# Optimization experiments

Measured on AMD Instinct MI355X. Metric: run time of the kernel, lower is better.

## Reference

```python
import jax, jax.numpy as jnp
import numpy as np

HEADS = 16
HEAD_DIM = 64

def setup_inputs() -> dict:
    key = jax.random.key(0)
    ks = jax.random.split(key, 5)
    S, B, H = 1024, 4, 1024
    scale = 1.0 / np.sqrt(H)
    return {
        "hidden_states": jax.random.normal(ks[0], (S, B, H), jnp.float32),
        "attention_mask": jnp.zeros((B * HEADS, 1, S), jnp.float32),
        "Wq": jax.random.normal(ks[1], (H, H), jnp.float32) * scale,
        "bq": jnp.zeros((H,), jnp.float32),
        "Wk": jax.random.normal(ks[2], (H, H), jnp.float32) * scale,
        "bk": jnp.zeros((H,), jnp.float32),
        "Wv": jax.random.normal(ks[3], (H, H), jnp.float32) * scale,
        "bv": jnp.zeros((H,), jnp.float32),
    }

def reference(hidden_states, attention_mask, Wq, bq, Wk, bk, Wv, bv):
    S, B, H = hidden_states.shape
    d = HEAD_DIM
    inv_sqrt_d = 1.0 / np.sqrt(d)
    # QKV projections (torch Linear: x @ W.T + b)
    q = hidden_states @ Wq.T + bq  # (S, B, H)
    k = hidden_states @ Wk.T + bk
    v = hidden_states @ Wv.T + bv
    # (S, B*heads, d) -> (B*heads, S, d)
    q = q.reshape(S, B * HEADS, d).transpose(1, 0, 2)
    k = k.reshape(S, B * HEADS, d).transpose(1, 0, 2)
    v = v.reshape(S, B * HEADS, d).transpose(1, 0, 2)
    # SDDMM: scaled scores + additive mask -> (B*heads, S, S)
    scores = jnp.einsum('nsd,ntd->nst', q, k) * inv_sqrt_d + attention_mask
    probs = jax.nn.softmax(scores, axis=-1)
    # AV bmm -> (B*heads, S, d); note: dropout in source is seeded but never applied
    ctx = jnp.einsum('nst,ntd->nsd', probs, v)
    # back to (S, B, hidden)
    ctx = ctx.transpose(1, 0, 2).reshape(S, B, H)
    return ctx
```

## Files before the change

kernel.cpp:

```cpp
#include <hip/hip_runtime.h>
#include <hip/hip_bf16.h>
#include <math.h>

#define S_LEN 1024
#define BATCH 4
#define HID 1024
#define NHEADS 16
#define DHEAD 64
#define NTOT 64
#define M_ROWS 4096

typedef unsigned short u16;
typedef unsigned int u32;
typedef __bf16 bf16x8 __attribute__((ext_vector_type(8)));
typedef float f32x4 __attribute__((ext_vector_type(4)));

__device__ __forceinline__ u16 f2bf(float x) {
    __hip_bfloat16 h = __float2bfloat16(x);
    return *(u16*)&h;
}

__device__ __forceinline__ float fexp2(float x) {
#if __has_builtin(__builtin_amdgcn_exp2f)
    return __builtin_amdgcn_exp2f(x);
#else
    return __expf(x * 0.6931471805599453f);
#endif
}

__device__ __forceinline__ u32 cvtpk(float a, float b) {
    u32 r;
    asm("v_cvt_pk_bf16_f32 %0, %1, %2" : "=v"(r) : "v"(a), "v"(b));
    return r;
}

__device__ __forceinline__ void pl16swap(u32& a, u32& b) {
    asm("v_permlane16_swap_b32 %0, %1" : "+v"(a), "+v"(b));
}

__device__ __forceinline__ void gll16(const u16* g, u16* l) {
    __builtin_amdgcn_global_load_lds(
        (const __attribute__((address_space(1))) u32*)g,
        (__attribute__((address_space(3))) u32*)l, 16, 0, 0);
}

__global__ __launch_bounds__(256) void cvt_all(
    const float* __restrict__ X, const float* __restrict__ wq,
    const float* __restrict__ wk, const float* __restrict__ wv,
    u16* __restrict__ Xb, u16* __restrict__ Wb)
{
    const int bid = blockIdx.x;
    const float* src;
    u16* dst;
    size_t off;
    if (bid < 4096) {
        src = X; dst = Xb; off = (size_t)bid * 1024;
    } else {
        const int wb = bid - 4096;
        const int which = wb >> 10;
        src = (which == 0) ? wq : (which == 1) ? wk : wv;
        dst = Wb + (size_t)which * HID * HID;
        off = (size_t)(wb & 1023) * 1024;
    }
    const size_t idx = off + threadIdx.x * 4;
    float4 x = *(const float4*)(src + idx);
    *(ushort4*)(dst + idx) = make_ushort4(f2bf(x.x), f2bf(x.y), f2bf(x.z), f2bf(x.w));
}

__global__ __launch_bounds__(256, 3) void qkv_mfma(
    const u16* __restrict__ Xb, const u16* __restrict__ Wb,
    const float* __restrict__ bq, const float* __restrict__ bk,
    const float* __restrict__ bv,
    u16* __restrict__ Qb, u16* __restrict__ Kb, u16* __restrict__ VT)
{
    const int m0 = blockIdx.x * 128;
    const int n0 = blockIdx.y * 128;
    const int which = blockIdx.z;

    __shared__ __align__(16) u16 As[128 * 64];
    __shared__ __align__(16) u16 Bs[128 * 64];

    const int tid = threadIdx.x;
    const int lane = tid & 63;
    const int w = tid >> 6;
    const int wm = w & 1, wn = w >> 1;
    const int quad = lane >> 4;
    const int l15 = lane & 15;
    const int r7 = l15 & 7;

    const u16* W = Wb + (size_t)which * HID * HID;

    f32x4 acc[4][4];
    #pragma unroll
    for (int i = 0; i < 4; ++i)
        #pragma unroll
        for (int j = 0; j < 4; ++j)
            #pragma unroll
            for (int r = 0; r < 4; ++r) acc[i][j][r] = 0.0f;

    const int srow = lane >> 3;
    const int scg  = ((lane & 7) ^ srow) * 8;

    for (int k0 = 0; k0 < HID; k0 += 64) {
        #pragma unroll
        for (int c = 0; c < 4; ++c) {
            const int seg = w * 4 + c;
            const int row = seg * 8 + srow;
            gll16(Xb + (size_t)(m0 + row) * HID + k0 + scg, As + seg * 512);
            gll16(W  + (size_t)(n0 + row) * HID + k0 + scg, Bs + seg * 512);
        }
        __syncthreads();

        #pragma unroll
        for (int kk = 0; kk < 2; ++kk) {
            const int xo = ((kk * 4 + quad) ^ r7) * 8;
            bf16x8 af[4], bf[4];
            #pragma unroll
            for (int i = 0; i < 4; ++i)
                af[i] = *(const bf16x8*)(As + (wm * 64 + i * 16 + l15) * 64 + xo);
            #pragma unroll
            for (int j = 0; j < 4; ++j)
                bf[j] = *(const bf16x8*)(Bs + (wn * 64 + j * 16 + l15) * 64 + xo);
            #pragma unroll
            for (int i = 0; i < 4; ++i)
                #pragma unroll
                for (int j = 0; j < 4; ++j)
                    acc[i][j] = __builtin_amdgcn_mfma_f32_16x16x32_bf16(
                        af[i], bf[j], acc[i][j], 0, 0, 0);
        }
        __syncthreads();
    }

    const float* bias = (which == 0) ? bq : (which == 1) ? bk : bv;
    #pragma unroll
    for (int j = 0; j < 4; ++j) {
        const int o = n0 + wn * 64 + j * 16 + l15;
        const float bias_v = bias[o];
        const int head = o >> 6, d = o & 63;
        #pragma unroll
        for (int i = 0; i < 4; ++i) {
            const int mbase = m0 + wm * 64 + i * 16 + quad * 4;
            const int s = mbase >> 2;
            #pragma unroll
            for (int r = 0; r < 4; ++r) {
                const int n = r * NHEADS + head;
                const u16 hv = f2bf(acc[i][j][r] + bias_v);
                if (which == 0)
                    Qb[((size_t)n * S_LEN + s) * DHEAD + d] = hv;
                else if (which == 1)
                    Kb[((size_t)n * S_LEN + s) * DHEAD + d] = hv;
                else
                    VT[(size_t)n * (DHEAD * S_LEN) + (size_t)d * S_LEN + s] = hv;
            }
        }
    }
}

__global__ __launch_bounds__(256, 2) void attn_mfma(
    const u16* __restrict__ Qb, const u16* __restrict__ Kb,
    const u16* __restrict__ VT, const float* __restrict__ mask,
    float* __restrict__ out)
{
    const int bid = blockIdx.x;
    const int swz = (bid & 7) * 64 + (bid >> 3);
    const int n = swz >> 3;
    const int s0 = (swz & 7) * 128;
    const int b = n >> 4, head = n & 15;

    __shared__ __align__(16) char smem[69632];
    u16* Kbuf = (u16*)smem;
    u16* Vbuf = (u16*)(smem + 32768);
    float* Ms = (float*)(smem + 65536);
    float* Of = (float*)smem;

    const int tid = threadIdx.x;
    const int lane = tid & 63;
    const int w = tid >> 6;
    const int quad = lane >> 4;
    const int l15 = lane & 15;
    const int r7 = l15 & 7;
    const size_t nbase = (size_t)n * S_LEN * DHEAD;

    const float LOG2E = 1.44269504f;
    const float SCL2  = 0.18033688f;
    const float MOFF  = -23.0831099f;

    const int xs0 = ((quad ^ r7) * 8);
    const int xs1 = (((4 + quad) ^ r7) * 8);
    const int qperm = ((quad & 1) << 1) | (quad >> 1);
    const int xv0 = ((qperm ^ r7) * 8);
    const int xv1 = (((4 + qperm) ^ r7) * 8);

    const int srow = lane >> 3;
    const int scg  = (lane & 7) ^ (srow & 7);

    {
        float4 mv = *(const float4*)(mask + (size_t)n * S_LEN + tid * 4);
        Ms[tid * 4 + 0] = fmaf(mv.x, LOG2E, MOFF);
        Ms[tid * 4 + 1] = fmaf(mv.y, LOG2E, MOFF);
        Ms[tid * 4 + 2] = fmaf(mv.z, LOG2E, MOFF);
        Ms[tid * 4 + 3] = fmaf(mv.w, LOG2E, MOFF);
    }

    bf16x8 qf[2][2];
    #pragma unroll
    for (int mi = 0; mi < 2; ++mi)
        #pragma unroll
        for (int st = 0; st < 2; ++st)
            qf[mi][st] = *(const bf16x8*)(Qb + nbase +
                (size_t)(s0 + w * 32 + mi * 16 + l15) * 64 + st * 32 + quad * 8);

    f32x4 O[2][4];
    float l_lane[2];
    #pragma unroll
    for (int mi = 0; mi < 2; ++mi) {
        l_lane[mi] = 0.0f;
        #pragma unroll
        for (int jt = 0; jt < 4; ++jt)
            #pragma unroll
            for (int r = 0; r < 4; ++r) O[mi][jt][r] = 0.0f;
    }

    {
        #pragma unroll
        for (int h = 0; h < 2; ++h) {
            #pragma unroll
            for (int c = 0; c < 2; ++c) {
                const int seg = w * 2 + c;
                const int row = seg * 8 + srow;
                gll16(Kb + nbase + (size_t)(h * 64 + row) * 64 + scg * 8,
                      Kbuf + h * 4096 + seg * 512);
                gll16(VT + nbase + (size_t)row * S_LEN + h * 64 + scg * 8,
                      Vbuf + h * 4096 + seg * 512);
            }
        }
    }
    __syncthreads();

    u32 pw[2][2][2][4];

    for (int it = 0; it < 8; ++it) {
        const int t0 = it * 128;
        const u16* kb = Kbuf + (it & 1) * 8192;
        const u16* vb = Vbuf + (it & 1) * 8192;

        if (it < 7) {
            u16* kd = Kbuf + ((it + 1) & 1) * 8192;
            u16* vd = Vbuf + ((it + 1) & 1) * 8192;
            const int t0n = t0 + 128;
            #pragma unroll
            for (int h = 0; h < 2; ++h) {
                #pragma unroll
                for (int c = 0; c < 2; ++c) {
                    const int seg = w * 2 + c;
                    const int row = seg * 8 + srow;
                    gll16(Kb + nbase + (size_t)(t0n + h * 64 + row) * 64 + scg * 8,
                          kd + h * 4096 + seg * 512);
                    gll16(VT + nbase + (size_t)row * S_LEN + t0n + h * 64 + scg * 8,
                          vd + h * 4096 + seg * 512);
                }
            }
        }

        #pragma unroll
        for (int h = 0; h < 2; ++h) {
            const u16* kbh = kb + h * 4096;

            f32x4 sc[2][4];
            #pragma unroll
            for (int mi = 0; mi < 2; ++mi)
                #pragma unroll
                for (int j = 0; j < 4; ++j)
                    #pragma unroll
                    for (int r = 0; r < 4; ++r) sc[mi][j][r] = 0.0f;

            __builtin_amdgcn_s_setprio(1);
            #pragma unroll
            for (int st = 0; st < 2; ++st) {
                const int xo = st ? xs1 : xs0;
                bf16x8 kf[4];
                #pragma unroll
                for (int j = 0; j < 4; ++j)
                    kf[j] = *(const bf16x8*)(kbh + (j * 16 + l15) * 64 + xo);
                #pragma unroll
                for (int mi = 0; mi < 2; ++mi)
                    #pragma unroll
                    for (int j = 0; j < 4; ++j)
                        sc[mi][j] = __builtin_amdgcn_mfma_f32_16x16x32_bf16(
                            kf[j], qf[mi][st], sc[mi][j], 0, 0, 0);
            }
            __builtin_amdgcn_s_setprio(0);

            float4 mb4[4];
            #pragma unroll
            for (int j = 0; j < 4; ++j)
                mb4[j] = *(const float4*)(Ms + t0 + h * 64 + j * 16 + quad * 4);

            #pragma unroll
            for (int mi = 0; mi < 2; ++mi) {
                float pj[4][4];
                #pragma unroll
                for (int j = 0; j < 4; ++j) {
                    pj[j][0] = fexp2(fmaf(sc[mi][j][0], SCL2, mb4[j].x));
                    pj[j][1] = fexp2(fmaf(sc[mi][j][1], SCL2, mb4[j].y));
                    pj[j][2] = fexp2(fmaf(sc[mi][j][2], SCL2, mb4[j].z));
                    pj[j][3] = fexp2(fmaf(sc[mi][j][3], SCL2, mb4[j].w));
                    l_lane[mi] += (pj[j][0] + pj[j][1]) + (pj[j][2] + pj[j][3]);
                }
                u32 W00 = cvtpk(pj[0][0], pj[0][1]), W01 = cvtpk(pj[0][2], pj[0][3]);
                u32 W10 = cvtpk(pj[1][0], pj[1][1]), W11 = cvtpk(pj[1][2], pj[1][3]);
                u32 W20 = cvtpk(pj[2][0], pj[2][1]), W21 = cvtpk(pj[2][2], pj[2][3]);
                u32 W30 = cvtpk(pj[3][0], pj[3][1]), W31 = cvtpk(pj[3][2], pj[3][3]);
                pl16swap(W00, W10); pl16swap(W01, W11);
                pl16swap(W20, W30); pl16swap(W21, W31);
                pw[mi][h][0][0] = W00; pw[mi][h][0][1] = W01;
                pw[mi][h][0][2] = W10; pw[mi][h][0][3] = W11;
                pw[mi][h][1][0] = W20; pw[mi][h][1][1] = W21;
                pw[mi][h][1][2] = W30; pw[mi][h][1][3] = W31;
            }
        }

        __builtin_amdgcn_s_setprio(1);
        #pragma unroll
        for (int h = 0; h < 2; ++h) {
            const u16* vbh = vb + h * 4096;
            #pragma unroll
            for (int st = 0; st < 2; ++st) {
                const int xo = st ? xv1 : xv0;
                bf16x8 vf[4];
                #pragma unroll
                for (int jt = 0; jt < 4; ++jt)
                    vf[jt] = *(const bf16x8*)(vbh + (jt * 16 + l15) * 64 + xo);
                #pragma unroll
                for (int mi = 0; mi < 2; ++mi) {
                    union { u32 wds[4]; bf16x8 v; } pu;
                    pu.wds[0] = pw[mi][h][st][0]; pu.wds[1] = pw[mi][h][st][1];
                    pu.wds[2] = pw[mi][h][st][2]; pu.wds[3] = pw[mi][h][st][3];
                    #pragma unroll
                    for (int jt = 0; jt < 4; ++jt)
                        O[mi][jt] = __builtin_amdgcn_mfma_f32_16x16x32_bf16(
                            vf[jt], pu.v, O[mi][jt], 0, 0, 0);
                }
            }
        }
        __builtin_amdgcn_s_setprio(0);

        __syncthreads();
    }

    float inv_l[2];
    #pragma unroll
    for (int mi = 0; mi < 2; ++mi) {
        float l = l_lane[mi];
        l += __shfl_xor(l, 16);
        l += __shfl_xor(l, 32);
        inv_l[mi] = 1.0f / l;
    }
    __syncthreads();

    #pragma unroll
    for (int mi = 0; mi < 2; ++mi) {
        const int q = w * 32 + mi * 16 + l15;
        #pragma unroll
        for (int jt = 0; jt < 4; ++jt)
            #pragma unroll
            for (int r = 0; r < 4; ++r)
                Of[q * 72 + jt * 16 + quad * 4 + r] = O[mi][jt][r] * inv_l[mi];
    }
    __syncthreads();

    const int tx = tid & 15, ty = tid >> 4;
    #pragma unroll
    for (int p = 0; p < 8; ++p) {
        const int q = p * 16 + ty;
        float4 v = *(const float4*)(Of + q * 72 + tx * 4);
        *(float4*)(out + (size_t)(s0 + q) * (BATCH * HID) + (size_t)b * HID +
                   head * DHEAD + tx * 4) = v;
    }
}

extern "C" void kernel_launch(void* const* d_in, const int* in_sizes, int n_in,
                              void* d_out, int out_size, void* d_ws, size_t ws_size,
                              hipStream_t stream)
{
    const float* X    = (const float*)d_in[0];
    const float* mask = (const float*)d_in[1];
    const float* Wq   = (const float*)d_in[2];
    const float* bq   = (const float*)d_in[3];
    const float* Wk   = (const float*)d_in[4];
    const float* bk   = (const float*)d_in[5];
    const float* Wv   = (const float*)d_in[6];
    const float* bv   = (const float*)d_in[7];
    float* out = (float*)d_out;

    const size_t MX = (size_t)M_ROWS * HID;
    const size_t MW = (size_t)HID * HID;
    u16* wsp = (u16*)d_ws;
    u16* Xb = wsp;
    u16* Wb = Xb + MX;
    u16* Qb = Wb + 3 * MW;
    u16* Kb = Qb + MX;
    u16* VT = Kb + MX;

    cvt_all<<<dim3(4096 + 3072), 256, 0, stream>>>(X, Wq, Wk, Wv, Xb, Wb);
    qkv_mfma<<<dim3(M_ROWS / 128, HID / 128, 3), 256, 0, stream>>>(
        Xb, Wb, bq, bk, bv, Qb, Kb, VT);
    attn_mfma<<<dim3(S_LEN / 128 * NTOT), 256, 0, stream>>>(Qb, Kb, VT, mask, out);
}
```

Before: 146.1 us.

## Load V fragments directly from global into registers instead of LDS staging

Drops the LDS double buffer for V^T and has each lane load its V MFMA fragments straight from global memory at the start of each key tile. It also interleaves the PV MFMAs per half-tile with the score computation, so the P registers live for a shorter span. This frees about 32 KB of shared memory per block and removes the V LDS reads. In exchange, every wave reloads the same V data from global or L2 with no prefetch distance, and 16 extra bf16x8 registers per lane may raise register pressure and expose load latency.

Result: slower. 157.5 us (+7.8%).

```diff
diff --git a/kernel.cpp b/kernel.cpp
--- a/kernel.cpp
+++ b/kernel.cpp
@@ -167,10 +167,9 @@
     const int s0 = (swz & 7) * 128;
     const int b = n >> 4, head = n & 15;
 
-    __shared__ __align__(16) char smem[69632];
+    __shared__ __align__(16) char smem[36864];
     u16* Kbuf = (u16*)smem;
-    u16* Vbuf = (u16*)(smem + 32768);
-    float* Ms = (float*)(smem + 65536);
+    float* Ms = (float*)(smem + 32768);
     float* Of = (float*)smem;
 
     const int tid = threadIdx.x;
@@ -188,8 +187,6 @@
     const int xs0 = ((quad ^ r7) * 8);
     const int xs1 = (((4 + quad) ^ r7) * 8);
     const int qperm = ((quad & 1) << 1) | (quad >> 1);
-    const int xv0 = ((qperm ^ r7) * 8);
-    const int xv1 = (((4 + qperm) ^ r7) * 8);
 
     const int srow = lane >> 3;
     const int scg  = (lane & 7) ^ (srow & 7);
@@ -230,23 +227,28 @@
                 const int row = seg * 8 + srow;
                 gll16(Kb + nbase + (size_t)(h * 64 + row) * 64 + scg * 8,
                       Kbuf + h * 4096 + seg * 512);
-                gll16(VT + nbase + (size_t)row * S_LEN + h * 64 + scg * 8,
-                      Vbuf + h * 4096 + seg * 512);
             }
         }
     }
     __syncthreads();
-
-    u32 pw[2][2][2][4];
 
     for (int it = 0; it < 8; ++it) {
         const int t0 = it * 128;
         const u16* kb = Kbuf + (it & 1) * 8192;
-        const u16* vb = Vbuf + (it & 1) * 8192;
+
+        bf16x8 vgl[2][2][4];
+        #pragma unroll
+        for (int h = 0; h < 2; ++h)
+            #pragma unroll
+            for (int st = 0; st < 2; ++st)
+                #pragma unroll
+                for (int jt = 0; jt < 4; ++jt)
+                    vgl[h][st][jt] = *(const bf16x8*)(VT + nbase +
+                        (size_t)(jt * 16 + l15) * S_LEN +
+                        t0 + h * 64 + (st * 4 + qperm) * 8);
 
         if (it < 7) {
             u16* kd = Kbuf + ((it + 1) & 1) * 8192;
-            u16* vd = Vbuf + ((it + 1) & 1) * 8192;
             const int t0n = t0 + 128;
             #pragma unroll
             for (int h = 0; h < 2; ++h) {
@@ -256,8 +258,6 @@
                     const int row = seg * 8 + srow;
                     gll16(Kb + nbase + (size_t)(t0n + h * 64 + row) * 64 + scg * 8,
                           kd + h * 4096 + seg * 512);
-                    gll16(VT + nbase + (size_t)row * S_LEN + t0n + h * 64 + scg * 8,
-                          vd + h * 4096 + seg * 512);
                 }
             }
         }
@@ -296,6 +296,7 @@
             for (int j = 0; j < 4; ++j)
                 mb4[j] = *(const float4*)(Ms + t0 + h * 64 + j * 16 + quad * 4);
 
+            u32 pw[2][2][4];
             #pragma unroll
             for (int mi = 0; mi < 2; ++mi) {
                 float pj[4][4];
@@ -313,37 +314,27 @@
                 u32 W30 = cvtpk(pj[3][0], pj[3][1]), W31 = cvtpk(pj[3][2], pj[3][3]);
                 pl16swap(W00, W10); pl16swap(W01, W11);
                 pl16swap(W20, W30); pl16swap(W21, W31);
-                pw[mi][h][0][0] = W00; pw[mi][h][0][1] = W01;
-                pw[mi][h][0][2] = W10; pw[mi][h][0][3] = W11;
-                pw[mi][h][1][0] = W20; pw[mi][h][1][1] = W21;
-                pw[mi][h][1][2] = W30; pw[mi][h][1][3] = W31;
+                pw[mi][0][0] = W00; pw[mi][0][1] = W01;
+                pw[mi][0][2] = W10; pw[mi][0][3] = W11;
+                pw[mi][1][0] = W20; pw[mi][1][1] = W21;
+                pw[mi][1][2] = W30; pw[mi][1][3] = W31;
             }
-        }
-
-        __builtin_amdgcn_s_setprio(1);
-        #pragma unroll
-        for (int h = 0; h < 2; ++h) {
-            const u16* vbh = vb + h * 4096;
-            #pragma unroll
-            for (int st = 0; st < 2; ++st) {
-                const int xo = st ? xv1 : xv0;
-                bf16x8 vf[4];
-                #pragma unroll
-                for (int jt = 0; jt < 4; ++jt)
-                    vf[jt] = *(const bf16x8*)(vbh + (jt * 16 + l15) * 64 + xo);
+
+            __builtin_amdgcn_s_setprio(1);
+            #pragma unroll
+            for (int st = 0; st < 2; ++st)
                 #pragma unroll
                 for (int mi = 0; mi < 2; ++mi) {
                     union { u32 wds[4]; bf16x8 v; } pu;
-                    pu.wds[0] = pw[mi][h][st][0]; pu.wds[1] = pw[mi][h][st][1];
-                    pu.wds[2] = pw[mi][h][st][2]; pu.wds[3] = pw[mi][h][st][3];
+                    pu.wds[0] = pw[mi][st][0]; pu.wds[1] = pw[mi][st][1];
+                    pu.wds[2] = pw[mi][st][2]; pu.wds[3] = pw[mi][st][3];
                     #pragma unroll
                     for (int jt = 0; jt < 4; ++jt)
                         O[mi][jt] = __builtin_amdgcn_mfma_f32_16x16x32_bf16(
-                            vf[jt], pu.v, O[mi][jt], 0, 0, 0);
+                            vgl[h][st][jt], pu.v, O[mi][jt], 0, 0, 0);
                 }
-            }
-        }
-        __builtin_amdgcn_s_setprio(0);
+            __builtin_amdgcn_s_setprio(0);
+        }
 
         __syncthreads();
     }
```

## Double-buffer QKV GEMM LDS tiles and widen N tile to fuse projections

Applied to the files above, without the earlier changes.

The QKV projection kernel now treats the three weight matrices as one 3072-wide output and uses 128x192 tiles. Each block covers 192 output columns, which may straddle the Q/K/V boundary, so the bias and output pointer are selected per column. LDS tiles are double-buffered, so the next k-slice loads while MFMAs run on the current one, and one barrier per iteration is removed. The cost is a larger accumulator set and twice the LDS, which lowers the occupancy target from 3 to 2 blocks per CU, and fewer blocks are launched (512 instead of 768).

Result: slower. 149.6 us (+2.4%).

```diff
diff --git a/kernel.cpp b/kernel.cpp
--- a/kernel.cpp
+++ b/kernel.cpp
@@ -67,18 +67,17 @@
     *(ushort4*)(dst + idx) = make_ushort4(f2bf(x.x), f2bf(x.y), f2bf(x.z), f2bf(x.w));
 }
 
-__global__ __launch_bounds__(256, 3) void qkv_mfma(
+__global__ __launch_bounds__(256, 2) void qkv_mfma(
     const u16* __restrict__ Xb, const u16* __restrict__ Wb,
     const float* __restrict__ bq, const float* __restrict__ bk,
     const float* __restrict__ bv,
     u16* __restrict__ Qb, u16* __restrict__ Kb, u16* __restrict__ VT)
 {
     const int m0 = blockIdx.x * 128;
-    const int n0 = blockIdx.y * 128;
-    const int which = blockIdx.z;
-
-    __shared__ __align__(16) u16 As[128 * 64];
-    __shared__ __align__(16) u16 Bs[128 * 64];
+    const int n0 = blockIdx.y * 192;
+
+    __shared__ __align__(16) u16 As[2][128 * 64];
+    __shared__ __align__(16) u16 Bs[2][192 * 64];
 
     const int tid = threadIdx.x;
     const int lane = tid & 63;
@@ -88,55 +87,77 @@
     const int l15 = lane & 15;
     const int r7 = l15 & 7;
 
-    const u16* W = Wb + (size_t)which * HID * HID;
-
-    f32x4 acc[4][4];
+    f32x4 acc[4][6];
     #pragma unroll
     for (int i = 0; i < 4; ++i)
         #pragma unroll
-        for (int j = 0; j < 4; ++j)
+        for (int j = 0; j < 6; ++j)
             #pragma unroll
             for (int r = 0; r < 4; ++r) acc[i][j][r] = 0.0f;
 
     const int srow = lane >> 3;
     const int scg  = ((lane & 7) ^ srow) * 8;
 
-    for (int k0 = 0; k0 < HID; k0 += 64) {
-        #pragma unroll
-        for (int c = 0; c < 4; ++c) {
-            const int seg = w * 4 + c;
-            const int row = seg * 8 + srow;
-            gll16(Xb + (size_t)(m0 + row) * HID + k0 + scg, As + seg * 512);
-            gll16(W  + (size_t)(n0 + row) * HID + k0 + scg, Bs + seg * 512);
-        }
-        __syncthreads();
+    #pragma unroll
+    for (int c = 0; c < 4; ++c) {
+        const int seg = w * 4 + c;
+        gll16(Xb + (size_t)(m0 + seg * 8 + srow) * HID + scg, As[0] + seg * 512);
+    }
+    #pragma unroll
+    for (int c = 0; c < 6; ++c) {
+        const int seg = w * 6 + c;
+        gll16(Wb + (size_t)(n0 + seg * 8 + srow) * HID + scg, Bs[0] + seg * 512);
+    }
+    __syncthreads();
+
+    for (int t = 0; t < 16; ++t) {
+        const int cur = t & 1;
+
+        if (t < 15) {
+            const int nxt = cur ^ 1;
+            const int k1 = (t + 1) * 64;
+            #pragma unroll
+            for (int c = 0; c < 4; ++c) {
+                const int seg = w * 4 + c;
+                gll16(Xb + (size_t)(m0 + seg * 8 + srow) * HID + k1 + scg,
+                      As[nxt] + seg * 512);
+            }
+            #pragma unroll
+            for (int c = 0; c < 6; ++c) {
+                const int seg = w * 6 + c;
+                gll16(Wb + (size_t)(n0 + seg * 8 + srow) * HID + k1 + scg,
+                      Bs[nxt] + seg * 512);
+            }
+        }
 
         #pragma unroll
         for (int kk = 0; kk < 2; ++kk) {
             const int xo = ((kk * 4 + quad) ^ r7) * 8;
-            bf16x8 af[4], bf[4];
+            bf16x8 af[4], bf[6];
             #pragma unroll
             for (int i = 0; i < 4; ++i)
-                af[i] = *(const bf16x8*)(As + (wm * 64 + i * 16 + l15) * 64 + xo);
-            #pragma unroll
-            for (int j = 0; j < 4; ++j)
-                bf[j] = *(const bf16x8*)(Bs + (wn * 64 + j * 16 + l15) * 64 + xo);
+                af[i] = *(const bf16x8*)(As[cur] + (wm * 64 + i * 16 + l15) * 64 + xo);
+            #pragma unroll
+            for (int j = 0; j < 6; ++j)
+                bf[j] = *(const bf16x8*)(Bs[cur] + (wn * 96 + j * 16 + l15) * 64 + xo);
             #pragma unroll
             for (int i = 0; i < 4; ++i)
                 #pragma unroll
-                for (int j = 0; j < 4; ++j)
+                for (int j = 0; j < 6; ++j)
                     acc[i][j] = __builtin_amdgcn_mfma_f32_16x16x32_bf16(
                         af[i], bf[j], acc[i][j], 0, 0, 0);
         }
         __syncthreads();
     }
 
-    const float* bias = (which == 0) ? bq : (which == 1) ? bk : bv;
-    #pragma unroll
-    for (int j = 0; j < 4; ++j) {
-        const int o = n0 + wn * 64 + j * 16 + l15;
-        const float bias_v = bias[o];
-        const int head = o >> 6, d = o & 63;
+    #pragma unroll
+    for (int j = 0; j < 6; ++j) {
+        const int o = n0 + wn * 96 + j * 16 + l15;
+        const int which = o >> 10;
+        const int hd = o & 1023;
+        const float* bias = (which == 0) ? bq : (which == 1) ? bk : bv;
+        const float bias_v = bias[hd];
+        const int head = hd >> 6, d = hd & 63;
         #pragma unroll
         for (int i = 0; i < 4; ++i) {
             const int mbase = m0 + wm * 64 + i * 16 + quad * 4;
@@ -403,7 +424,7 @@
     u16* VT = Kb + MX;
 
     cvt_all<<<dim3(4096 + 3072), 256, 0, stream>>>(X, Wq, Wk, Wv, Xb, Wb);
-    qkv_mfma<<<dim3(M_ROWS / 128, HID / 128, 3), 256, 0, stream>>>(
+    qkv_mfma<<<dim3(M_ROWS / 128, 3072 / 192), 256, 0, stream>>>(
         Xb, Wb, bq, bk, bv, Qb, Kb, VT);
     attn_mfma<<<dim3(S_LEN / 128 * NTOT), 256, 0, stream>>>(Qb, Kb, VT, mask, out);
 }
```

## Double-buffer QKV GEMM LDS tiles with K=32 stages to overlap loads

Applied to the files above, without the earlier changes.

The QKV projection GEMM now uses two LDS buffers of K-depth 32 instead of a single K=64 buffer. The next tile's global-to-LDS loads are issued before computing on the current one, leaving one barrier per iteration. The swizzle is reworked for the 32-wide rows. This aims to hide global load latency behind MFMA work, at the cost of twice as many iterations and barriers with half the MFMA work between them.

Result: slower. 150.2 us (+2.8%).

```diff
diff --git a/kernel.cpp b/kernel.cpp
--- a/kernel.cpp
+++ b/kernel.cpp
@@ -77,8 +77,8 @@
     const int n0 = blockIdx.y * 128;
     const int which = blockIdx.z;
 
-    __shared__ __align__(16) u16 As[128 * 64];
-    __shared__ __align__(16) u16 Bs[128 * 64];
+    __shared__ __align__(16) u16 As[2][128 * 32];
+    __shared__ __align__(16) u16 Bs[2][128 * 32];
 
     const int tid = threadIdx.x;
     const int lane = tid & 63;
@@ -86,7 +86,6 @@
     const int wm = w & 1, wn = w >> 1;
     const int quad = lane >> 4;
     const int l15 = lane & 15;
-    const int r7 = l15 & 7;
 
     const u16* W = Wb + (size_t)which * HID * HID;
 
@@ -98,36 +97,50 @@
             #pragma unroll
             for (int r = 0; r < 4; ++r) acc[i][j][r] = 0.0f;
 
-    const int srow = lane >> 3;
-    const int scg  = ((lane & 7) ^ srow) * 8;
-
-    for (int k0 = 0; k0 < HID; k0 += 64) {
-        #pragma unroll
-        for (int c = 0; c < 4; ++c) {
-            const int seg = w * 4 + c;
-            const int row = seg * 8 + srow;
-            gll16(Xb + (size_t)(m0 + row) * HID + k0 + scg, As + seg * 512);
-            gll16(W  + (size_t)(n0 + row) * HID + k0 + scg, Bs + seg * 512);
-        }
-        __syncthreads();
-
-        #pragma unroll
-        for (int kk = 0; kk < 2; ++kk) {
-            const int xo = ((kk * 4 + quad) ^ r7) * 8;
-            bf16x8 af[4], bf[4];
-            #pragma unroll
-            for (int i = 0; i < 4; ++i)
-                af[i] = *(const bf16x8*)(As + (wm * 64 + i * 16 + l15) * 64 + xo);
+    const int srow = lane >> 2;
+    const int scol = ((lane & 3) ^ ((lane >> 3) & 3)) * 8;
+
+    const int xq = (quad ^ ((l15 >> 1) & 3)) * 8;
+
+    #pragma unroll
+    for (int c = 0; c < 2; ++c) {
+        const int seg = w * 2 + c;
+        const int row = seg * 16 + srow;
+        gll16(Xb + (size_t)(m0 + row) * HID + scol, As[0] + seg * 512);
+        gll16(W  + (size_t)(n0 + row) * HID + scol, Bs[0] + seg * 512);
+    }
+    __syncthreads();
+
+    for (int t = 0; t < 32; ++t) {
+        const int cur = t & 1;
+
+        if (t < 31) {
+            const int k1 = (t + 1) * 32;
+            #pragma unroll
+            for (int c = 0; c < 2; ++c) {
+                const int seg = w * 2 + c;
+                const int row = seg * 16 + srow;
+                gll16(Xb + (size_t)(m0 + row) * HID + k1 + scol,
+                      As[cur ^ 1] + seg * 512);
+                gll16(W  + (size_t)(n0 + row) * HID + k1 + scol,
+                      Bs[cur ^ 1] + seg * 512);
+            }
+        }
+
+        bf16x8 af[4], bf[4];
+        #pragma unroll
+        for (int i = 0; i < 4; ++i)
+            af[i] = *(const bf16x8*)(As[cur] + (wm * 64 + i * 16 + l15) * 32 + xq);
+        #pragma unroll
+        for (int j = 0; j < 4; ++j)
+            bf[j] = *(const bf16x8*)(Bs[cur] + (wn * 64 + j * 16 + l15) * 32 + xq);
+        #pragma unroll
+        for (int i = 0; i < 4; ++i)
             #pragma unroll
             for (int j = 0; j < 4; ++j)
-                bf[j] = *(const bf16x8*)(Bs + (wn * 64 + j * 16 + l15) * 64 + xo);
-            #pragma unroll
-            for (int i = 0; i < 4; ++i)
-                #pragma unroll
-                for (int j = 0; j < 4; ++j)
-                    acc[i][j] = __builtin_amdgcn_mfma_f32_16x16x32_bf16(
-                        af[i], bf[j], acc[i][j], 0, 0, 0);
-        }
+                acc[i][j] = __builtin_amdgcn_mfma_f32_16x16x32_bf16(
+                    af[i], bf[j], acc[i][j], 0, 0, 0);
+
         __syncthreads();
     }
 
```
